# Optimization experiments

Hardware: AMD Instinct MI355X
Metric: run time of the kernel (lower is better)

The kernel has to match this reference:

```python
import jax, jax.numpy as jnp
from jax import lax
import numpy as np
import math

B_SZ, SEQ, D_MODEL = 2, 2048, 2048
D_INNER, D_STATE, D_CONV, HEADS, P, CHUNK = 4096, 128, 4, 64, 64, 128
CONV_DIM = D_INNER + 2 * D_STATE
D_IN_PROJ = 2 * D_INNER + 2 * D_STATE + HEADS


def setup_inputs() -> dict:
    key = jax.random.key(0)
    ks = jax.random.split(key, 6)
    hidden_states = jax.random.normal(ks[0], (B_SZ, SEQ, D_MODEL), jnp.float32)
    W_in = jax.random.normal(ks[1], (D_IN_PROJ, D_MODEL), jnp.float32) * 0.02
    W_conv = jax.random.normal(ks[2], (CONV_DIM, 1, D_CONV), jnp.float32) * 0.2
    b_conv = jnp.zeros((CONV_DIM,), jnp.float32)
    A_log = jnp.log(jnp.arange(1, HEADS + 1, dtype=jnp.float32))
    D = jnp.ones((HEADS,), jnp.float32)
    # dt_bias init as in the torch module
    dt = jnp.exp(jax.random.uniform(ks[3], (HEADS,)) * (math.log(0.1) - math.log(0.001)) + math.log(0.001))
    dt = jnp.clip(dt, 1e-4, None)
    dt_bias = dt + jnp.log(-jnp.expm1(-dt))
    norm_weight = jnp.ones((D_INNER,), jnp.float32)
    W_out = jax.random.normal(ks[4], (D_MODEL, D_INNER), jnp.float32) * 0.02
    return {"hidden_states": hidden_states, "W_in": W_in, "W_conv": W_conv, "b_conv": b_conv,
            "A_log": A_log, "D": D, "dt_bias": dt_bias, "norm_weight": norm_weight, "W_out": W_out}


def _mamba2_core(hidden_states, W_in, W_conv, b_conv, A_log, D, dt_bias, norm_weight, W_out):
    Bsz, L, _ = hidden_states.shape
    NC = L // CHUNK
    zxbcdt = hidden_states @ W_in.T                         # [B,L,d_in_proj]
    z = zxbcdt[..., :D_INNER]
    xBC = zxbcdt[..., D_INNER:D_INNER + CONV_DIM]
    dt = zxbcdt[..., -HEADS:]
    # causal depthwise conv1d over sequence
    xc = jnp.swapaxes(xBC, 1, 2)                            # [B,C,L]
    xc = lax.conv_general_dilated(xc, W_conv, (1,), [(D_CONV - 1, 0)],
                                  feature_group_count=CONV_DIM,
                                  dimension_numbers=('NCH', 'OIH', 'NCH'))
    xc = xc + b_conv[None, :, None]
    xBC = jax.nn.silu(jnp.swapaxes(xc, 1, 2))               # [B,L,conv_dim]
    x = xBC[..., :D_INNER]
    Bm = xBC[..., D_INNER:D_INNER + D_STATE]                # num_groups=1
    Cm = xBC[..., -D_STATE:]
    dt = jax.nn.softplus(dt + dt_bias)                      # [B,L,H]; dt_limit (0,inf) is a no-op
    A = -jnp.exp(A_log)                                     # [H]
    # --- chunked SSD scan (chunk_size = CHUNK), same math as torch_ssm ---
    xch = x.reshape(Bsz, NC, CHUNK, HEADS, P)
    dtc = dt.reshape(Bsz, NC, CHUNK, HEADS)
    Bc = Bm.reshape(Bsz, NC, CHUNK, D_STATE)
    Cc = Cm.reshape(Bsz, NC, CHUNK, D_STATE)
    u = xch * dtc[..., None]                                # [b,c,l,h,p]
    dA = dtc * A                                            # [b,c,l,h]
    dA_cs = jnp.cumsum(dA, axis=2)                          # [b,c,l,h]
    # within-chunk causal attention-like term
    seg = dA_cs[:, :, :, None, :] - dA_cs[:, :, None, :, :] # [b,c,l,s,h]
    mask = jnp.tril(jnp.ones((CHUNK, CHUNK), bool))
    Lmat = jnp.exp(jnp.where(mask[None, None, :, :, None], seg, -jnp.inf))
    CB = jnp.einsum('bcln,bcsn->bcls', Cc, Bc)
    M = CB[..., None] * Lmat                                # [b,c,l,s,h]
    Y_diag = jnp.einsum('bclsh,bcshp->bclhp', M, u)
    # per-chunk final states
    decay_states = jnp.exp(dA_cs[:, :, -1:, :] - dA_cs)     # [b,c,l,h]
    states = jnp.einsum('bcln,bclh,bclhp->bchpn', Bc, decay_states, u)
    chunk_decay = jnp.exp(dA_cs[:, :, -1, :])               # [b,c,h]
    # inter-chunk recurrence over NC chunks
    def step(h, inp):
        st, cd = inp                                        # [b,h,p,n], [b,h]
        h_new = h * cd[:, :, None, None] + st
        return h_new, h                                     # emit state at chunk start
    sts = jnp.moveaxis(states, 1, 0)
    cds = jnp.moveaxis(chunk_decay, 1, 0)
    h0 = jnp.zeros((Bsz, HEADS, P, D_STATE), hidden_states.dtype)
    _, h_starts = lax.scan(step, h0, (sts, cds))
    h_starts = jnp.moveaxis(h_starts, 0, 1)                 # [b,c,h,p,n]
    state_decay_out = jnp.exp(dA_cs)                        # [b,c,l,h]
    Y_off = jnp.einsum('bcln,bclh,bchpn->bclhp', Cc, state_decay_out, h_starts)
    Y = Y_diag + Y_off + D[None, None, None, :, None] * xch
    y = Y.reshape(Bsz, L, D_INNER)
    # gated RMSNorm (gate first, then norm; group_size == d_inner)
    yg = y * jax.nn.silu(z)
    var = jnp.mean(yg * yg, axis=-1, keepdims=True)
    y = yg * lax.rsqrt(var + 1e-5) * norm_weight
    return y @ W_out.T


def reference(hidden_states, W_in, W_conv, b_conv, A_log, D, dt_bias, norm_weight, W_out):
    return _mamba2_core(hidden_states, W_in, W_conv, b_conv, A_log, D, dt_bias, norm_weight, W_out)
```

## Files before the change

### kernel.cpp

```cpp
#include <hip/hip_runtime.h>
#include <hip/hip_bf16.h>
#include <stdint.h>

typedef __bf16 bf16;
typedef __bf16 bf16x8 __attribute__((ext_vector_type(8)));
typedef __bf16 bf16x4 __attribute__((ext_vector_type(4)));
typedef float f32x4v __attribute__((ext_vector_type(4)));

#define SEQ    2048
#define DMODEL 2048
#define DI     4096
#define NH     64
#define PDIM   64
#define CHUNKL 128
#define NCH    16
#define CONVD  4352
#define DPROJ  8512
#define ZLD    8704
#define NTOK   4096
#define LP     136

__device__ __forceinline__ float sigmoid_f(float x){ return 1.f/(1.f+expf(-x)); }
__device__ __forceinline__ float silu_f(float x){ return x*sigmoid_f(x); }
__device__ __forceinline__ float softplus_f(float x){ return x > 20.f ? x : log1pf(expf(x)); }

__global__ __launch_bounds__(256) void cvt_all_kernel(const float* __restrict__ hs,
                                                      const float* __restrict__ W_in,
                                                      const float* __restrict__ W_out,
                                                      bf16* __restrict__ hsb,
                                                      bf16* __restrict__ winb,
                                                      bf16* __restrict__ woutb){
    int blk = blockIdx.x;
    if (blk < 8192){
        int i = (blk*256 + threadIdx.x)*4;
        float4 v = *(const float4*)&hs[i];
        bf16x4 o; o[0]=(bf16)v.x; o[1]=(bf16)v.y; o[2]=(bf16)v.z; o[3]=(bf16)v.w;
        *(bf16x4*)&hsb[i] = o;
    } else if (blk < 25600){
        int i = ((blk-8192)*256 + threadIdx.x)*4;
        int r = i >> 11;
        bf16x4 o;
        if (r < DPROJ){
            float4 v = *(const float4*)&W_in[i];
            o[0]=(bf16)v.x; o[1]=(bf16)v.y; o[2]=(bf16)v.z; o[3]=(bf16)v.w;
        } else {
            o[0]=(bf16)0.f; o[1]=(bf16)0.f; o[2]=(bf16)0.f; o[3]=(bf16)0.f;
        }
        *(bf16x4*)&winb[i] = o;
    } else {
        int i = ((blk-25600)*256 + threadIdx.x)*4;
        float4 v = *(const float4*)&W_out[i];
        bf16x4 o; o[0]=(bf16)v.x; o[1]=(bf16)v.y; o[2]=(bf16)v.z; o[3]=(bf16)v.w;
        *(bf16x4*)&woutb[i] = o;
    }
}

#define READ_AF(BUFP, QM, AF)                                                          \
    {                                                                                  \
        _Pragma("unroll")                                                              \
        for (int i=0;i<4;i++)                                                          \
            _Pragma("unroll")                                                          \
            for (int k2=0;k2<2;k2++)                                                   \
                AF[i][k2] = *(const bf16x8*)&(BUFP)[aoff[i][k2] + (QM)*8192];          \
    }

#define READ_B(BUFP, QN, BFR)                                                          \
    {                                                                                  \
        _Pragma("unroll")                                                              \
        for (int nf=0;nf<2;nf++)                                                       \
            _Pragma("unroll")                                                          \
            for (int k2=0;k2<2;k2++)                                                   \
                BFR[nf][k2] = *(const bf16x8*)&(BUFP)[boff[nf][k2] + (QN)*8192];       \
    }

#define MMA_QA(AF, QM, QN, BFR)                                                        \
    {                                                                                  \
        __builtin_amdgcn_s_setprio(1);                                                 \
        _Pragma("unroll")                                                              \
        for (int i=0;i<4;i++)                                                          \
            _Pragma("unroll")                                                          \
            for (int nf=0;nf<2;nf++)                                                   \
                _Pragma("unroll")                                                      \
                for (int k2=0;k2<2;k2++)                                               \
                    acc[(QM)*4+i][(QN)*2+nf] = __builtin_amdgcn_mfma_f32_16x16x32_bf16( \
                        AF[i][k2], BFR[nf][k2], acc[(QM)*4+i][(QN)*2+nf], 0,0,0);      \
        __builtin_amdgcn_s_setprio(0);                                                 \
    }

#define SBAR() do { __builtin_amdgcn_sched_barrier(0);                                 \
                    __builtin_amdgcn_s_barrier();                                      \
                    asm volatile("s_waitcnt lgkmcnt(0)" ::: "memory");                 \
                    __builtin_amdgcn_sched_barrier(0); } while(0)

__global__ __launch_bounds__(512) void gemm1_kernel(const bf16* __restrict__ A,
                                                    const bf16* __restrict__ Bmat,
                                                    bf16* __restrict__ Cz,
                                                    float* __restrict__ tpart,
                                                    int NXB, int NYB, int K){
    __shared__ __align__(16) bf16 lds[2][2*16384];
    const int tid  = threadIdx.x;
    const int w    = tid >> 6;
    const int lane = tid & 63;
    const int wm   = w >> 2, wn = w & 3;
    const int bid  = blockIdx.x;

    int aoff[4][2], boff[2][2];
    #pragma unroll
    for (int i=0;i<4;i++)
        #pragma unroll
        for (int k2=0;k2<2;k2++){
            int ra0 = wm*64 + i*16 + (lane&15);
            int slot = (k2*4 + (lane>>4)) ^ (ra0&7);
            aoff[i][k2] = ra0*64 + slot*8;
        }
    #pragma unroll
    for (int nf=0;nf<2;nf++)
        #pragma unroll
        for (int k2=0;k2<2;k2++){
            int rb0 = wn*32 + nf*16 + (lane&15);
            int slot = (k2*4 + (lane>>4)) ^ (rb0&7);
            boff[nf][k2] = 16384 + rb0*64 + slot*8;
        }
    const int er = (lane>>4)*4, ec = lane&15;

    if (bid < 256){
        int kz  = bid >> 6;
        int t64 = bid & 63;
        const int tn2 = 8192 + (t64 & 3)*128;
        const int tm2 = (t64 >> 2)*256;
        const int kt0 = kz*8;

        const bf16* srcA2[2][2];
        const bf16* srcB2[2];
        #pragma unroll
        for (int r0h=0;r0h<2;r0h++)
            #pragma unroll
            for (int i=0;i<2;i++){
                int lr = r0h*128 + i*64 + (tid>>3);
                int growA = tm2 + ((lr>>6)&1)*128 + (lr>>7)*64 + (lr&63);
                int gslot = (tid&7) ^ (lr&7);
                srcA2[r0h][i] = A + (long)growA*K + gslot*8;
            }
        #pragma unroll
        for (int i=0;i<2;i++){
            int lr = i*64 + (tid>>3);
            int gslot = (tid&7) ^ (lr&7);
            srcB2[i] = Bmat + (long)(tn2 + lr)*K + gslot*8;
        }
        auto stA = [&](int buf, int t, int r0h){
            long koff = (long)(kt0 + t)*64;
            #pragma unroll
            for (int i=0;i<2;i++){
                bf16* dst = &lds[buf][0] + (size_t)(r0h*128 + i*64 + w*8)*64;
                __builtin_amdgcn_global_load_lds(
                    (const __attribute__((address_space(1))) void*)(srcA2[r0h][i] + koff),
                    (__attribute__((address_space(3))) void*)dst, 16, 0, 0);
            }
        };
        auto stB = [&](int buf, int t){
            long koff = (long)(kt0 + t)*64;
            #pragma unroll
            for (int i=0;i<2;i++){
                bf16* dst = &lds[buf][16384] + (size_t)(i*64 + w*8)*64;
                __builtin_amdgcn_global_load_lds(
                    (const __attribute__((address_space(1))) void*)(srcB2[i] + koff),
                    (__attribute__((address_space(3))) void*)dst, 16, 0, 0);
            }
        };

        f32x4v acc2[8][2];
        #pragma unroll
        for (int i=0;i<8;i++)
            #pragma unroll
            for (int j=0;j<2;j++) acc2[i][j] = {0.f,0.f,0.f,0.f};
        bf16x8 af[4][2], af1[4][2], bfr0[2][2];

        stA(0,0,0); stA(0,0,1); stB(0,0);
        __syncthreads();
        int cur = 0;
        for (int t=0; t<8; ++t){
            int nxt = cur ^ 1;
            const bf16* bufc = &lds[cur][0];
            if (t+1 < 8){ stA(nxt,t+1,0); stA(nxt,t+1,1); stB(nxt,t+1); }
            READ_AF(bufc, 0, af)
            READ_AF(bufc, 1, af1)
            READ_B(bufc, 0, bfr0)
            #pragma unroll
            for (int i=0;i<4;i++)
                #pragma unroll
                for (int nf=0;nf<2;nf++)
                    #pragma unroll
                    for (int k2=0;k2<2;k2++)
                        acc2[i][nf] = __builtin_amdgcn_mfma_f32_16x16x32_bf16(
                            af[i][k2], bfr0[nf][k2], acc2[i][nf], 0,0,0);
            #pragma unroll
            for (int i=0;i<4;i++)
                #pragma unroll
                for (int nf=0;nf<2;nf++)
                    #pragma unroll
                    for (int k2=0;k2<2;k2++)
                        acc2[4+i][nf] = __builtin_amdgcn_mfma_f32_16x16x32_bf16(
                            af1[i][k2], bfr0[nf][k2], acc2[4+i][nf], 0,0,0);
            __syncthreads();
            cur = nxt;
        }
        #pragma unroll
        for (int mi=0;mi<8;mi++)
            #pragma unroll
            for (int nf=0;nf<2;nf++){
                long r0 = tm2 + wm*128 + mi*16 + er;
                int  c0 = tn2 + wn*32 + nf*16 + ec;
                #pragma unroll
                for (int j=0;j<4;j++)
                    tpart[((long)kz*4096 + (r0+j))*512 + (c0 - 8192)] = acc2[mi][nf][j];
            }
        return;
    }

    int bid2 = bid - 256;
    int wg   = (bid2 & 7)*64 + (bid2 >> 3);
    const int SW = 8;
    int sup = wg / (SW*NYB);
    int rr  = wg % (SW*NYB);
    int x0  = sup*SW;
    int wl  = (NXB - x0 < SW) ? (NXB - x0) : SW;
    int x   = x0 + rr % wl;
    int y   = rr / wl;
    const int tm = y*256, tn = x*256;
    const int KT = K >> 6;

    f32x4v acc[8][4];
    #pragma unroll
    for (int i=0;i<8;i++)
        #pragma unroll
        for (int j=0;j<4;j++) acc[i][j] = {0.f,0.f,0.f,0.f};
    bf16x8 af[4][2], af1[4][2];
    bf16x8 bfr0[2][2], bfr1[2][2];

    const bf16* srcA[2][2];
    const bf16* srcB[2][2];
    #pragma unroll
    for (int r0h=0;r0h<2;r0h++)
        #pragma unroll
        for (int i=0;i<2;i++){
            int lr = r0h*128 + i*64 + (tid>>3);
            int growA = tm + ((lr>>6)&1)*128 + (lr>>7)*64 + (lr&63);
            int growB = tn + ((lr>>5)&3)*64 + (lr>>7)*32 + (lr&31);
            int gslot = (tid&7) ^ (lr&7);
            srcA[r0h][i] = A + (long)growA*K + gslot*8;
            srcB[r0h][i] = Bmat + (long)growB*K + gslot*8;
        }

    auto stageA = [&](int buf, int t, int r0h){
        long koff = (long)t*64;
        #pragma unroll
        for (int i=0;i<2;i++){
            bf16* dst = &lds[buf][0] + (size_t)(r0h*128 + i*64 + w*8)*64;
            __builtin_amdgcn_global_load_lds(
                (const __attribute__((address_space(1))) void*)(srcA[r0h][i] + koff),
                (__attribute__((address_space(3))) void*)dst, 16, 0, 0);
        }
    };
    auto stageB = [&](int buf, int t, int r0h){
        long koff = (long)t*64;
        #pragma unroll
        for (int i=0;i<2;i++){
            bf16* dst = &lds[buf][16384] + (size_t)(r0h*128 + i*64 + w*8)*64;
            __builtin_amdgcn_global_load_lds(
                (const __attribute__((address_space(1))) void*)(srcB[r0h][i] + koff),
                (__attribute__((address_space(3))) void*)dst, 16, 0, 0);
        }
    };

    stageA(0, 0, 0); stageB(0, 0, 0); stageB(0, 0, 1); stageA(0, 0, 1);
    if (KT > 1){ stageA(1, 1, 0); stageB(1, 1, 0); stageB(1, 1, 1); }

    int cur = 0;
    for (int t = 0; t < KT; ++t){
        int nxt = cur ^ 1;
        const bf16* bufc = &lds[cur][0];
        if (t+1 < KT){ asm volatile("s_waitcnt vmcnt(6)" ::: "memory"); }
        else         { asm volatile("s_waitcnt vmcnt(0)" ::: "memory"); }
        __builtin_amdgcn_sched_barrier(0);
        __builtin_amdgcn_s_barrier();
        __builtin_amdgcn_sched_barrier(0);
        if (t+1 < KT) stageA(nxt, t+1, 1);
        READ_AF(bufc, 0, af)
        READ_AF(bufc, 1, af1)
        READ_B(bufc, 0, bfr0)
        READ_B(bufc, 1, bfr1)
        asm volatile("s_waitcnt lgkmcnt(0)" ::: "memory");
        __builtin_amdgcn_sched_barrier(0);
        MMA_QA(af, 0, 0, bfr0)
        MMA_QA(af, 0, 1, bfr1)
        __builtin_amdgcn_sched_barrier(0);
        __builtin_amdgcn_s_barrier();
        __builtin_amdgcn_sched_barrier(0);
        if (t+2 < KT){ stageA(cur, t+2, 0); stageB(cur, t+2, 0); stageB(cur, t+2, 1); }
        MMA_QA(af1, 1, 0, bfr0)
        MMA_QA(af1, 1, 1, bfr1)
        __builtin_amdgcn_sched_barrier(0);
        cur = nxt;
    }

    #pragma unroll
    for (int mi=0;mi<8;mi++)
        #pragma unroll
        for (int ni=0;ni<4;ni++){
            long r0 = tm + wm*128 + mi*16 + er;
            int  c0 = tn + wn*64 + ni*16 + ec;
            #pragma unroll
            for (int j=0;j<4;j++)
                Cz[(r0+j)*ZLD + c0] = (bf16)acc[mi][ni][j];
        }
}

__global__ __launch_bounds__(512) void gemm256x128_kernel(const bf16* __restrict__ A,
                                                          const bf16* __restrict__ Bmat,
                                                          float* __restrict__ C,
                                                          int NXB, int NYB, int K, int ldc){
    __shared__ __align__(16) bf16 lds[3][24576];
    const int tid  = threadIdx.x;
    const int w    = tid >> 6;
    const int lane = tid & 63;
    const int wm   = w >> 2, wn = w & 3;

    int bid = blockIdx.x, nb = gridDim.x;
    int wg = (bid & 7)*(nb >> 3) + (bid >> 3);
    const int SW = 8;
    int sup = wg / (SW*NYB);
    int rr  = wg % (SW*NYB);
    int x0  = sup*SW;
    int wl  = (NXB - x0 < SW) ? (NXB - x0) : SW;
    int x   = x0 + rr % wl;
    int y   = rr / wl;
    const int tm = y*256, tn = x*128;
    const int KT = K >> 6;

    f32x4v acc[8][2];
    #pragma unroll
    for (int i=0;i<8;i++)
        #pragma unroll
        for (int j=0;j<2;j++) acc[i][j] = {0.f,0.f,0.f,0.f};
    bf16x8 af[4][2], af1[4][2];
    bf16x8 bfr[2][2];

    const bf16* srcA[2][2];
    const bf16* srcB[2];
    #pragma unroll
    for (int r0h=0;r0h<2;r0h++)
        #pragma unroll
        for (int i=0;i<2;i++){
            int lr = r0h*128 + i*64 + (tid>>3);
            int growA = tm + ((lr>>6)&1)*128 + (lr>>7)*64 + (lr&63);
            int gslot = (tid&7) ^ (lr&7);
            srcA[r0h][i] = A + (long)growA*K + gslot*8;
        }
    #pragma unroll
    for (int i=0;i<2;i++){
        int lr = i*64 + (tid>>3);
        int gslot = (tid&7) ^ (lr&7);
        srcB[i] = Bmat + (long)(tn + lr)*K + gslot*8;
    }
    int aoff[4][2], boff[2][2];
    #pragma unroll
    for (int i=0;i<4;i++)
        #pragma unroll
        for (int k2=0;k2<2;k2++){
            int ra0 = wm*64 + i*16 + (lane&15);
            int slot = (k2*4 + (lane>>4)) ^ (ra0&7);
            aoff[i][k2] = ra0*64 + slot*8;
        }
    #pragma unroll
    for (int nf=0;nf<2;nf++)
        #pragma unroll
        for (int k2=0;k2<2;k2++){
            int rb0 = wn*32 + nf*16 + (lane&15);
            int slot = (k2*4 + (lane>>4)) ^ (rb0&7);
            boff[nf][k2] = 16384 + rb0*64 + slot*8;
        }

    auto stageA = [&](int buf, int t, int r0h){
        long koff = (long)t*64;
        #pragma unroll
        for (int i=0;i<2;i++){
            bf16* dst = &lds[buf][0] + (size_t)(r0h*128 + i*64 + w*8)*64;
            __builtin_amdgcn_global_load_lds(
                (const __attribute__((address_space(1))) void*)(srcA[r0h][i] + koff),
                (__attribute__((address_space(3))) void*)dst, 16, 0, 0);
        }
    };
    auto stageB = [&](int buf, int t){
        long koff = (long)t*64;
        #pragma unroll
        for (int i=0;i<2;i++){
            bf16* dst = &lds[buf][16384] + (size_t)(i*64 + w*8)*64;
            __builtin_amdgcn_global_load_lds(
                (const __attribute__((address_space(1))) void*)(srcB[i] + koff),
                (__attribute__((address_space(3))) void*)dst, 16, 0, 0);
        }
    };

    stageA(0, 0, 0); stageA(0, 0, 1); stageB(0, 0);
    if (KT > 1){ stageA(1, 1, 0); stageA(1, 1, 1); stageB(1, 1); }
    asm volatile("s_waitcnt vmcnt(6)" ::: "memory");
    __builtin_amdgcn_s_barrier();

    int cur = 0;
    for (int t = 0; t < KT; ++t){
        int stb = cur + 2; if (stb >= 3) stb -= 3;
        const bf16* bufc = &lds[cur][0];
        READ_AF(bufc, 0, af)
        READ_AF(bufc, 1, af1)
        READ_B(bufc, 0, bfr)
        if (t+2 < KT){ stageA(stb, t+2, 0); stageA(stb, t+2, 1); }
        SBAR();
        MMA_QA(af, 0, 0, bfr)
        if (t+2 < KT){
            stageB(stb, t+2);
            asm volatile("s_waitcnt vmcnt(6)" ::: "memory");
        } else {
            asm volatile("s_waitcnt vmcnt(0)" ::: "memory");
        }
        SBAR();
        MMA_QA(af1, 1, 0, bfr)
        cur = (cur == 2) ? 0 : cur + 1;
    }

    const int er = (lane>>4)*4, ec = lane&15;
    #pragma unroll
    for (int mi=0;mi<8;mi++)
        #pragma unroll
        for (int ni=0;ni<2;ni++){
            long r0 = tm + wm*128 + mi*16 + er;
            int  c0 = tn + wn*32 + ni*16 + ec;
            #pragma unroll
            for (int j=0;j<4;j++)
                C[(r0+j)*ldc + c0] = acc[mi][ni][j];
        }
}

__global__ __launch_bounds__(256) void tailreduce_kernel(const float* __restrict__ p,
                                                         bf16* __restrict__ zx,
                                                         float* __restrict__ dtf){
    long i = ((long)blockIdx.x*256 + threadIdx.x)*4;
    int r = (int)(i >> 9);
    int c = (int)(i & 511);
    const long Q = (long)4096*512;
    float4 a  = *(const float4*)&p[i];
    float4 b  = *(const float4*)&p[i+Q];
    float4 cc = *(const float4*)&p[i+2*Q];
    float4 d  = *(const float4*)&p[i+3*Q];
    float s0 = a.x+b.x+cc.x+d.x, s1 = a.y+b.y+cc.y+d.y;
    float s2 = a.z+b.z+cc.z+d.z, s3 = a.w+b.w+cc.w+d.w;
    bf16x4 o; o[0]=(bf16)s0; o[1]=(bf16)s1; o[2]=(bf16)s2; o[3]=(bf16)s3;
    *(bf16x4*)&zx[(long)r*ZLD + 8192 + c] = o;
    int col = 8192 + c;
    float sv[4] = {s0,s1,s2,s3};
    #pragma unroll
    for (int j=0;j<4;j++){
        int cj = col + j;
        if (cj >= 8448 && cj < 8512) dtf[(long)r*64 + (cj-8448)] = sv[j];
    }
}

__global__ __launch_bounds__(256) void mid1_kernel(const bf16* __restrict__ zx,
                                                   const float* __restrict__ Wc,
                                                   const float* __restrict__ bc,
                                                   const float* __restrict__ dtf,
                                                   const float* __restrict__ A_log,
                                                   const float* __restrict__ dt_bias,
                                                   bf16* __restrict__ xc,
                                                   float* __restrict__ dtv,
                                                   float* __restrict__ dacs,
                                                   float* __restrict__ cdec){
    int blk = blockIdx.x;
    if (blk < 2560){
        int by = blk/5, bx = blk%5;
        int c4 = bx*256 + threadIdx.x;
        if (c4 >= 1088) return;
        int ch = c4*4;
        int b = by >> 8, t0 = (by & 255)*8;
        float4 tap[4];
        #pragma unroll
        for (int e=0;e<4;e++) tap[e] = *(const float4*)&Wc[(ch+e)*4];
        float4 bq = *(const float4*)&bc[ch];
        float bca[4] = {bq.x, bq.y, bq.z, bq.w};
        const bf16* col = zx + (long)(b*SEQ)*ZLD + 4096 + ch;
        bf16x4 v[11];
        #pragma unroll
        for (int k=0;k<11;k++){
            int t = t0 - 3 + k;
            if (t >= 0) v[k] = *(const bf16x4*)&col[(long)t*ZLD];
            else { v[k][0]=(bf16)0.f; v[k][1]=(bf16)0.f; v[k][2]=(bf16)0.f; v[k][3]=(bf16)0.f; }
        }
        #pragma unroll
        for (int j=0;j<8;j++){
            bf16x4 o;
            #pragma unroll
            for (int e=0;e<4;e++){
                float acc = bca[e] + (float)v[j][e]*tap[e].x + (float)v[j+1][e]*tap[e].y
                                   + (float)v[j+2][e]*tap[e].z + (float)v[j+3][e]*tap[e].w;
                o[e] = (bf16)silu_f(acc);
            }
            *(bf16x4*)&xc[(long)(b*SEQ + t0 + j)*CONVD + ch] = o;
        }
    } else {
        int wid  = ((blk-2560)*256 + threadIdx.x) >> 6;
        int lane = threadIdx.x & 63;
        int h  = wid & 63, bc2 = wid >> 6;
        int b  = bc2 >> 4,  c  = bc2 & 15;
        float Ah   = -expf(A_log[h]);
        float bias = dt_bias[h];
        long tok0 = (long)(b*SEQ + c*CHUNKL);
        int l0 = lane*2;
        float d0 = softplus_f(dtf[(tok0+l0)*64 + h] + bias);
        float d1 = softplus_f(dtf[(tok0+l0+1)*64 + h] + bias);
        float s = (d0 + d1)*Ah;
        #pragma unroll
        for (int off=1; off<64; off<<=1){
            float t = __shfl_up(s, off, 64);
            if (lane >= off) s += t;
        }
        long base_h = (long)wid*128;
        float cs1 = s;
        float cs0 = s - d1*Ah;
        dtv[base_h+l0]   = d0;  dtv[base_h+l0+1]  = d1;
        dacs[base_h+l0]  = cs0; dacs[base_h+l0+1] = cs1;
        if (lane == 63) cdec[wid] = expf(cs1);
    }
}

__global__ __launch_bounds__(256) void cb_mfma_kernel(const bf16* __restrict__ xc,
                                                      float* __restrict__ cb,
                                                      bf16* __restrict__ BT){
    __shared__ __align__(16) bf16 A1[128*LP];
    __shared__ __align__(16) bf16 B1[128*LP];
    int blk = blockIdx.x;  int b = blk>>4, c = blk&15;
    int tid = threadIdx.x;
    const int w = tid >> 6, lane = tid & 63;
    long tok0 = (long)(b*SEQ + c*CHUNKL);
    int l = tid>>1, n0 = (tid&1)*64;
    const bf16* crow = xc + tok0*CONVD + (long)l*CONVD;
    #pragma unroll
    for (int v=0;v<8;v++){
        *(bf16x8*)&A1[l*LP + n0 + v*8] = *(const bf16x8*)&crow[4224 + n0 + v*8];
        *(bf16x8*)&B1[l*LP + n0 + v*8] = *(const bf16x8*)&crow[4096 + n0 + v*8];
    }
    __syncthreads();
    f32x4v acc[2][8];
    #pragma unroll
    for (int mi=0;mi<2;mi++)
        #pragma unroll
        for (int ni=0;ni<8;ni++) acc[mi][ni] = {0.f,0.f,0.f,0.f};
    #pragma unroll
    for (int kk=0; kk<128; kk+=32){
        bf16x8 afr[2], bfr2[8];
        #pragma unroll
        for (int mi=0;mi<2;mi++)
            afr[mi] = *(const bf16x8*)&A1[(w*32 + mi*16 + (lane&15))*LP + kk + (lane>>4)*8];
        #pragma unroll
        for (int ni=0;ni<8;ni++)
            bfr2[ni] = *(const bf16x8*)&B1[(ni*16 + (lane&15))*LP + kk + (lane>>4)*8];
        #pragma unroll
        for (int mi=0;mi<2;mi++)
            #pragma unroll
            for (int ni=0;ni<8;ni++)
                acc[mi][ni] = __builtin_amdgcn_mfma_f32_16x16x32_bf16(afr[mi], bfr2[ni], acc[mi][ni], 0,0,0);
    }
    float* out = cb + (long)blk*16384;
    #pragma unroll
    for (int mi=0;mi<2;mi++)
        #pragma unroll
        for (int ni=0;ni<8;ni++){
            int r0 = w*32 + mi*16 + (lane>>4)*4;
            int c0 = ni*16 + (lane&15);
            #pragma unroll
            for (int j=0;j<4;j++) out[(long)(r0+j)*128 + c0] = acc[mi][ni][j];
        }
    {
        int n = tid>>1, s0 = (tid&1)*64;
        bf16* btp = BT + (long)blk*16384 + (long)n*128 + s0;
        #pragma unroll
        for (int v=0;v<8;v++){
            bf16x8 o;
            #pragma unroll
            for (int e=0;e<8;e++) o[e] = B1[(s0+v*8+e)*LP + n];
            *(bf16x8*)&btp[v*8] = o;
        }
    }
}

__global__ __launch_bounds__(256) void states_mfma_kernel(const bf16* __restrict__ xc,
                                                          const bf16* __restrict__ BT,
                                                          const float* __restrict__ dtv,
                                                          const float* __restrict__ dacs,
                                                          bf16* __restrict__ states){
    __shared__ __align__(16) bf16 A1[64*LP];
    __shared__ __align__(16) bf16 B1[128*LP];
    __shared__ float wgtl[128];
    int blk = blockIdx.x;
    int h = blk & 63, bc = blk >> 6;
    int b = bc >> 4, c = bc & 15;
    int tid = threadIdx.x;
    const int w = tid >> 6, lane = tid & 63;
    long tok0 = (long)(b*SEQ + c*CHUNKL);
    long base_h = (long)blk*128;
    float cs_last = dacs[base_h + 127];
    if (tid < 128) wgtl[tid] = dtv[base_h+tid] * expf(cs_last - dacs[base_h+tid]);
    __syncthreads();
    #pragma unroll
    for (int t=0;t<4;t++){
        int l = (tid>>3) + t*32;
        int p0 = (tid&7)*8;
        bf16x8 xv = *(const bf16x8*)&xc[(tok0+l)*CONVD + h*64 + p0];
        float wv = wgtl[l];
        #pragma unroll
        for (int e=0;e<8;e++) A1[(p0+e)*LP + l] = (bf16)((float)xv[e]*wv);
    }
    {
        int n = tid>>1, l0 = (tid&1)*64;
        const bf16* btp = BT + (long)bc*16384 + (long)n*128 + l0;
        #pragma unroll
        for (int v=0;v<8;v++)
            *(bf16x8*)&B1[n*LP + l0 + v*8] = *(const bf16x8*)&btp[v*8];
    }
    __syncthreads();
    f32x4v acc[8];
    #pragma unroll
    for (int ni=0;ni<8;ni++) acc[ni] = {0.f,0.f,0.f,0.f};
    #pragma unroll
    for (int kk=0; kk<128; kk+=32){
        bf16x8 afr = *(const bf16x8*)&A1[(w*16 + (lane&15))*LP + kk + (lane>>4)*8];
        #pragma unroll
        for (int ni=0;ni<8;ni++){
            bf16x8 bfr2 = *(const bf16x8*)&B1[(ni*16 + (lane&15))*LP + kk + (lane>>4)*8];
            acc[ni] = __builtin_amdgcn_mfma_f32_16x16x32_bf16(afr, bfr2, acc[ni], 0,0,0);
        }
    }
    bf16* out = states + (long)blk*8192;
    #pragma unroll
    for (int ni=0;ni<8;ni++){
        int p0 = w*16 + (lane>>4)*4;
        int n  = ni*16 + (lane&15);
        #pragma unroll
        for (int j=0;j<4;j++) out[(long)(p0+j)*128 + n] = (bf16)acc[ni][j];
    }
}

__global__ __launch_bounds__(256) void scan_kernel(const bf16* __restrict__ states,
                                                   const float* __restrict__ cdec,
                                                   bf16* __restrict__ hst){
    long gid = (long)blockIdx.x*256 + threadIdx.x;
    int n = gid & 127;
    int p = (gid >> 7) & 63;
    int h = (gid >> 13) & 63;
    int b = (int)(gid >> 19);
    float hrun = 0.f;
    for (int c=0;c<16;c++){
        long idx = ((((long)(b*16 + c)*64 + h)*64 + p)*128) + n;
        hst[idx] = (bf16)hrun;
        hrun = hrun * cdec[(b*16+c)*64 + h] + (float)states[idx];
    }
}

__global__ __launch_bounds__(256) void yfused_kernel(const bf16* __restrict__ xc,
                                                     const float* __restrict__ cb,
                                                     const bf16* __restrict__ hst,
                                                     const float* __restrict__ dtv,
                                                     const float* __restrict__ dacs,
                                                     bf16* __restrict__ Ybf){
    __shared__ __align__(16) bf16 A1[128*LP];
    __shared__ __align__(16) bf16 B1[64*LP];
    __shared__ float csl[128];
    int blk = blockIdx.x;
    int h = blk & 63, bc = blk >> 6;
    int b = bc >> 4, c = bc & 15;
    int tid = threadIdx.x;
    const int w = tid >> 6, lane = tid & 63;
    long tok0 = (long)(b*SEQ + c*CHUNKL);
    long base_h = (long)blk*128;
    if (tid < 128) csl[tid] = dacs[base_h + tid];
    __syncthreads();
    {
        int l = tid>>1, s0 = (tid&1)*64;
        float el = csl[l];
        const float* cbrow = cb + (long)bc*16384 + (long)l*128 + s0;
        int jend = l - s0; if (jend > 63) jend = 63;
        for (int j=0; j<=jend; j++)
            A1[l*LP + s0 + j] = (bf16)(cbrow[j]*expf(el - csl[s0+j]));
        for (int j=jend+1; j<64; j++)
            A1[l*LP + s0 + j] = (bf16)0.f;
    }
    #pragma unroll
    for (int t=0;t<4;t++){
        int s = (tid>>3) + t*32;
        int p0 = (tid&7)*8;
        bf16x8 xv = *(const bf16x8*)&xc[(tok0+s)*CONVD + h*64 + p0];
        float wv = dtv[base_h + s];
        #pragma unroll
        for (int e=0;e<8;e++) B1[(p0+e)*LP + s] = (bf16)((float)xv[e]*wv);
    }
    __syncthreads();
    f32x4v acc[2][4];
    #pragma unroll
    for (int mi=0;mi<2;mi++)
        #pragma unroll
        for (int ni=0;ni<4;ni++) acc[mi][ni] = {0.f,0.f,0.f,0.f};
    #pragma unroll
    for (int kk=0; kk<128; kk+=32){
        bf16x8 afr[2], bfr2[4];
        #pragma unroll
        for (int mi=0;mi<2;mi++)
            afr[mi] = *(const bf16x8*)&A1[(w*32 + mi*16 + (lane&15))*LP + kk + (lane>>4)*8];
        #pragma unroll
        for (int ni=0;ni<4;ni++)
            bfr2[ni] = *(const bf16x8*)&B1[(ni*16 + (lane&15))*LP + kk + (lane>>4)*8];
        #pragma unroll
        for (int mi=0;mi<2;mi++)
            #pragma unroll
            for (int ni=0;ni<4;ni++)
                acc[mi][ni] = __builtin_amdgcn_mfma_f32_16x16x32_bf16(afr[mi], bfr2[ni], acc[mi][ni], 0,0,0);
    }
    __syncthreads();
    {
        int l = tid>>1, n0 = (tid&1)*64;
        float e1 = expf(csl[l]);
        const bf16* crow = xc + (tok0+l)*CONVD + 4224;
        #pragma unroll
        for (int v=0;v<8;v++){
            bf16x8 cv = *(const bf16x8*)&crow[n0 + v*8];
            bf16x8 o;
            #pragma unroll
            for (int e=0;e<8;e++) o[e] = (bf16)((float)cv[e]*e1);
            *(bf16x8*)&A1[l*LP + n0 + v*8] = o;
        }
    }
    {
        int p = tid>>2, n0 = (tid&3)*32;
        const bf16* hrow = hst + (long)blk*8192 + (long)p*128 + n0;
        #pragma unroll
        for (int v=0;v<4;v++)
            *(bf16x8*)&B1[p*LP + n0 + v*8] = *(const bf16x8*)&hrow[v*8];
    }
    __syncthreads();
    #pragma unroll
    for (int kk=0; kk<128; kk+=32){
        bf16x8 afr[2], bfr2[4];
        #pragma unroll
        for (int mi=0;mi<2;mi++)
            afr[mi] = *(const bf16x8*)&A1[(w*32 + mi*16 + (lane&15))*LP + kk + (lane>>4)*8];
        #pragma unroll
        for (int ni=0;ni<4;ni++)
            bfr2[ni] = *(const bf16x8*)&B1[(ni*16 + (lane&15))*LP + kk + (lane>>4)*8];
        #pragma unroll
        for (int mi=0;mi<2;mi++)
            #pragma unroll
            for (int ni=0;ni<4;ni++)
                acc[mi][ni] = __builtin_amdgcn_mfma_f32_16x16x32_bf16(afr[mi], bfr2[ni], acc[mi][ni], 0,0,0);
    }
    #pragma unroll
    for (int mi=0;mi<2;mi++)
        #pragma unroll
        for (int ni=0;ni<4;ni++){
            int l0 = w*32 + mi*16 + (lane>>4)*4;
            int p  = ni*16 + (lane&15);
            #pragma unroll
            for (int j=0;j<4;j++)
                Ybf[(tok0 + l0 + j)*DI + h*64 + p] = (bf16)acc[mi][ni][j];
        }
}

__global__ __launch_bounds__(256) void gatenorm_kernel(const bf16* __restrict__ Ybf,
                                                       const bf16* __restrict__ zx,
                                                       const bf16* __restrict__ xc,
                                                       const float* __restrict__ Dp,
                                                       const float* __restrict__ nw,
                                                       bf16* __restrict__ ybn){
    __shared__ float red[4];
    int tok = blockIdx.x, tid = threadIdx.x;
    const bf16* yrow = Ybf + (long)tok*DI;
    const bf16* zrow = zx  + (long)tok*ZLD;
    const bf16* xrow = xc  + (long)tok*CONVD;
    float yg[16];
    float ss = 0.f;
    #pragma unroll
    for (int k=0;k<2;k++){
        int d = (tid + k*256)*8;
        bf16x8 yv = *(const bf16x8*)&yrow[d];
        bf16x8 zv = *(const bf16x8*)&zrow[d];
        bf16x8 xv = *(const bf16x8*)&xrow[d];
        float dh = Dp[d>>6];
        #pragma unroll
        for (int e=0;e<8;e++){
            float yy = (float)yv[e] + dh*(float)xv[e];
            float g = yy*silu_f((float)zv[e]);
            yg[k*8+e] = g;
            ss += g*g;
        }
    }
    #pragma unroll
    for (int off=32; off>0; off>>=1) ss += __shfl_down(ss, off, 64);
    if ((tid & 63) == 0) red[tid>>6] = ss;
    __syncthreads();
    float tot = red[0]+red[1]+red[2]+red[3];
    float scale = rsqrtf(tot/(float)DI + 1e-5f);
    #pragma unroll
    for (int k=0;k<2;k++){
        int d = (tid + k*256)*8;
        float4 w0 = *(const float4*)&nw[d];
        float4 w1 = *(const float4*)&nw[d+4];
        float wv[8] = {w0.x,w0.y,w0.z,w0.w,w1.x,w1.y,w1.z,w1.w};
        bf16x8 o;
        #pragma unroll
        for (int e=0;e<8;e++) o[e] = (bf16)(yg[k*8+e]*scale*wv[e]);
        *(bf16x8*)&ybn[(long)tok*DI + d] = o;
    }
}

extern "C" void kernel_launch(void* const* d_in, const int* in_sizes, int n_in,
                              void* d_out, int out_size, void* d_ws, size_t ws_size,
                              hipStream_t stream){
    const float* hs      = (const float*)d_in[0];
    const float* W_in    = (const float*)d_in[1];
    const float* W_conv  = (const float*)d_in[2];
    const float* b_conv  = (const float*)d_in[3];
    const float* A_log   = (const float*)d_in[4];
    const float* Dp      = (const float*)d_in[5];
    const float* dt_bias = (const float*)d_in[6];
    const float* nw      = (const float*)d_in[7];
    const float* W_out   = (const float*)d_in[8];
    float* out = (float*)d_out;

    char* ws = (char*)d_ws;
    const size_t OFF_ZX    = 0;
    const size_t OFF_DTF   = 71303168;
    const size_t OFF_XC    = 72351744;
    const size_t OFF_DTV   = 108003328;
    const size_t OFF_DACS  = 109051904;
    const size_t OFF_CDEC  = 110100480;
    const size_t OFF_CB    = 110108672;
    const size_t OFF_SLOTA = 112205824;
    const size_t OFF_SLOTB = 179314688;
    const size_t OFF_WOUTB = 212869120;

    bf16*  zx    = (bf16*)(ws + OFF_ZX);
    float* dtf   = (float*)(ws + OFF_DTF);
    bf16*  xc    = (bf16*)(ws + OFF_XC);
    float* dtv   = (float*)(ws + OFF_DTV);
    float* dacs  = (float*)(ws + OFF_DACS);
    float* cdec  = (float*)(ws + OFF_CDEC);
    float* cbuf  = (float*)(ws + OFF_CB);
    bf16*  hsb   = (bf16*)(ws + OFF_SLOTA);
    bf16*  winb  = (bf16*)(ws + OFF_SLOTA + 16777216);
    bf16*  states= (bf16*)(ws + OFF_SLOTA);
    bf16*  Ybf   = (bf16*)(ws + OFF_SLOTA);
    float* tpart = (float*)(ws + OFF_SLOTB);
    bf16*  BTb   = (bf16*)(ws + OFF_SLOTB);
    bf16*  hst   = (bf16*)(ws + OFF_SLOTB);
    bf16*  ybn   = (bf16*)(ws + OFF_SLOTB);
    bf16*  woutb = (bf16*)(ws + OFF_WOUTB);

    cvt_all_kernel<<<33792, 256, 0, stream>>>(hs, W_in, W_out, hsb, winb, woutb);

    gemm1_kernel<<<768, 512, 0, stream>>>(hsb, winb, zx, tpart, 32, 16, DMODEL);
    tailreduce_kernel<<<2048, 256, 0, stream>>>(tpart, zx, dtf);

    mid1_kernel<<<3072, 256, 0, stream>>>(zx, W_conv, b_conv, dtf, A_log, dt_bias,
                                          xc, dtv, dacs, cdec);
    cb_mfma_kernel<<<32, 256, 0, stream>>>(xc, cbuf, BTb);
    states_mfma_kernel<<<2048, 256, 0, stream>>>(xc, BTb, dtv, dacs, states);
    scan_kernel<<<4096, 256, 0, stream>>>(states, cdec, hst);
    yfused_kernel<<<2048, 256, 0, stream>>>(xc, cbuf, hst, dtv, dacs, Ybf);
    gatenorm_kernel<<<4096, 256, 0, stream>>>(Ybf, zx, xc, Dp, nw, ybn);

    gemm256x128_kernel<<<256, 512, 0, stream>>>(ybn, woutb, out, 16, 16, DI, DMODEL);
}
```

Measured before the change: 381.7 us.

## Replace split-K tail GEMM with uniform 128x256 tiled in-projection GEMM

The in-projection GEMM previously used 256x256 tiles for the main columns plus a split-K path for the 512-column tail, whose partial sums were reduced by a separate tail kernel. It is now one uniform kernel with 128x256 tiles, K-step 32, and a smaller LDS footprint allowing up to 4 blocks per CU. The dt columns go straight to dtf in fp32 from the epilogue. This removes the split-K partial-sum round trip and one kernel launch, but uses smaller tiles with less reuse per block and twice as many K iterations.

Result: slower. 407.5 us (+6.8%).

```diff
diff --git a/kernel.cpp b/kernel.cpp
--- a/kernel.cpp
+++ b/kernel.cpp
@@ -55,6 +55,128 @@
     }
 }
 
+__global__ __launch_bounds__(512, 4) void gemm1_kernel(const bf16* __restrict__ A,
+                                                       const bf16* __restrict__ Bmat,
+                                                       bf16* __restrict__ Cz,
+                                                       float* __restrict__ dtf,
+                                                       int NXB, int NYB, int K){
+    __shared__ __align__(16) bf16 lds[2][12288];
+    const int tid  = threadIdx.x;
+    const int w    = tid >> 6;
+    const int lane = tid & 63;
+    const int wm   = w >> 2, wn = w & 3;
+
+    int bid = blockIdx.x, nb = gridDim.x;
+    int wg  = (bid & 7)*(nb >> 3) + (bid >> 3);
+    const int SW = 8;
+    int sup = wg / (SW*NYB);
+    int rr  = wg % (SW*NYB);
+    int x0  = sup*SW;
+    int wl  = (NXB - x0 < SW) ? (NXB - x0) : SW;
+    int x   = x0 + rr % wl;
+    int y   = rr / wl;
+    const int tm = y*128, tn = x*256;
+    const int KT = K >> 5;
+
+    f32x4v acc[4][4];
+    #pragma unroll
+    for (int i=0;i<4;i++)
+        #pragma unroll
+        for (int j=0;j<4;j++) acc[i][j] = {0.f,0.f,0.f,0.f};
+    bf16x8 af[4], bfr[4];
+
+    const bf16* srcA1;
+    const bf16* srcB2[2];
+    {
+        int row = tid >> 2;
+        int gslot = (tid & 3) ^ ((row >> 1) & 3);
+        srcA1 = A + (long)(tm + row)*K + gslot*8;
+        #pragma unroll
+        for (int i=0;i<2;i++){
+            int rb = i*128 + row;
+            int gs = (tid & 3) ^ ((rb >> 1) & 3);
+            srcB2[i] = Bmat + (long)(tn + rb)*K + gs*8;
+        }
+    }
+    int aoff[4], boff[4];
+    #pragma unroll
+    for (int mi=0;mi<4;mi++){
+        int ra = wm*64 + mi*16 + (lane&15);
+        int slot = (lane>>4) ^ ((ra>>1)&3);
+        aoff[mi] = ra*32 + slot*8;
+    }
+    #pragma unroll
+    for (int ni=0;ni<4;ni++){
+        int rb = wn*64 + ni*16 + (lane&15);
+        int slot = (lane>>4) ^ ((rb>>1)&3);
+        boff[ni] = 4096 + rb*32 + slot*8;
+    }
+
+    auto stage = [&](int buf, int t){
+        long koff = (long)t*32;
+        {
+            bf16* dst = &lds[buf][0] + (size_t)w*512;
+            __builtin_amdgcn_global_load_lds(
+                (const __attribute__((address_space(1))) void*)(srcA1 + koff),
+                (__attribute__((address_space(3))) void*)dst, 16, 0, 0);
+        }
+        #pragma unroll
+        for (int i=0;i<2;i++){
+            bf16* dst = &lds[buf][4096] + (size_t)(i*4096 + w*512);
+            __builtin_amdgcn_global_load_lds(
+                (const __attribute__((address_space(1))) void*)(srcB2[i] + koff),
+                (__attribute__((address_space(3))) void*)dst, 16, 0, 0);
+        }
+    };
+
+    stage(0, 0);
+    if (KT > 1) stage(1, 1);
+
+    int cur = 0;
+    for (int t = 0; t < KT; ++t){
+        const bf16* bufc = &lds[cur][0];
+        if (t+1 < KT){ asm volatile("s_waitcnt vmcnt(3)" ::: "memory"); }
+        else         { asm volatile("s_waitcnt vmcnt(0)" ::: "memory"); }
+        __builtin_amdgcn_sched_barrier(0);
+        __builtin_amdgcn_s_barrier();
+        __builtin_amdgcn_sched_barrier(0);
+        #pragma unroll
+        for (int mi=0;mi<4;mi++) af[mi]  = *(const bf16x8*)&bufc[aoff[mi]];
+        #pragma unroll
+        for (int ni=0;ni<4;ni++) bfr[ni] = *(const bf16x8*)&bufc[boff[ni]];
+        asm volatile("s_waitcnt lgkmcnt(0)" ::: "memory");
+        __builtin_amdgcn_sched_barrier(0);
+        __builtin_amdgcn_s_setprio(1);
+        #pragma unroll
+        for (int mi=0;mi<4;mi++)
+            #pragma unroll
+            for (int ni=0;ni<4;ni++)
+                acc[mi][ni] = __builtin_amdgcn_mfma_f32_16x16x32_bf16(af[mi], bfr[ni], acc[mi][ni], 0,0,0);
+        __builtin_amdgcn_s_setprio(0);
+        __builtin_amdgcn_sched_barrier(0);
+        __builtin_amdgcn_s_barrier();
+        __builtin_amdgcn_sched_barrier(0);
+        if (t+2 < KT) stage(cur, t+2);
+        cur ^= 1;
+    }
+
+    const int er = (lane>>4)*4, ec = lane&15;
+    #pragma unroll
+    for (int mi=0;mi<4;mi++)
+        #pragma unroll
+        for (int ni=0;ni<4;ni++){
+            long r0 = tm + wm*64 + mi*16 + er;
+            int  c0 = tn + wn*64 + ni*16 + ec;
+            #pragma unroll
+            for (int j=0;j<4;j++){
+                float val = acc[mi][ni][j];
+                Cz[(r0+j)*ZLD + c0] = (bf16)val;
+                if (c0 >= 8448 && c0 < 8512)
+                    dtf[(r0+j)*64 + (c0 - 8448)] = val;
+            }
+        }
+}
+
 #define READ_AF(BUFP, QM, AF)                                                          \
     {                                                                                  \
         _Pragma("unroll")                                                              \
@@ -91,229 +213,6 @@
                     __builtin_amdgcn_s_barrier();                                      \
                     asm volatile("s_waitcnt lgkmcnt(0)" ::: "memory");                 \
                     __builtin_amdgcn_sched_barrier(0); } while(0)
-
-__global__ __launch_bounds__(512) void gemm1_kernel(const bf16* __restrict__ A,
-                                                    const bf16* __restrict__ Bmat,
-                                                    bf16* __restrict__ Cz,
-                                                    float* __restrict__ tpart,
-                                                    int NXB, int NYB, int K){
-    __shared__ __align__(16) bf16 lds[2][2*16384];
-    const int tid  = threadIdx.x;
-    const int w    = tid >> 6;
-    const int lane = tid & 63;
-    const int wm   = w >> 2, wn = w & 3;
-    const int bid  = blockIdx.x;
-
-    int aoff[4][2], boff[2][2];
-    #pragma unroll
-    for (int i=0;i<4;i++)
-        #pragma unroll
-        for (int k2=0;k2<2;k2++){
-            int ra0 = wm*64 + i*16 + (lane&15);
-            int slot = (k2*4 + (lane>>4)) ^ (ra0&7);
-            aoff[i][k2] = ra0*64 + slot*8;
-        }
-    #pragma unroll
-    for (int nf=0;nf<2;nf++)
-        #pragma unroll
-        for (int k2=0;k2<2;k2++){
-            int rb0 = wn*32 + nf*16 + (lane&15);
-            int slot = (k2*4 + (lane>>4)) ^ (rb0&7);
-            boff[nf][k2] = 16384 + rb0*64 + slot*8;
-        }
-    const int er = (lane>>4)*4, ec = lane&15;
-
-    if (bid < 256){
-        int kz  = bid >> 6;
-        int t64 = bid & 63;
-        const int tn2 = 8192 + (t64 & 3)*128;
-        const int tm2 = (t64 >> 2)*256;
-        const int kt0 = kz*8;
-
-        const bf16* srcA2[2][2];
-        const bf16* srcB2[2];
-        #pragma unroll
-        for (int r0h=0;r0h<2;r0h++)
-            #pragma unroll
-            for (int i=0;i<2;i++){
-                int lr = r0h*128 + i*64 + (tid>>3);
-                int growA = tm2 + ((lr>>6)&1)*128 + (lr>>7)*64 + (lr&63);
-                int gslot = (tid&7) ^ (lr&7);
-                srcA2[r0h][i] = A + (long)growA*K + gslot*8;
-            }
-        #pragma unroll
-        for (int i=0;i<2;i++){
-            int lr = i*64 + (tid>>3);
-            int gslot = (tid&7) ^ (lr&7);
-            srcB2[i] = Bmat + (long)(tn2 + lr)*K + gslot*8;
-        }
-        auto stA = [&](int buf, int t, int r0h){
-            long koff = (long)(kt0 + t)*64;
-            #pragma unroll
-            for (int i=0;i<2;i++){
-                bf16* dst = &lds[buf][0] + (size_t)(r0h*128 + i*64 + w*8)*64;
-                __builtin_amdgcn_global_load_lds(
-                    (const __attribute__((address_space(1))) void*)(srcA2[r0h][i] + koff),
-                    (__attribute__((address_space(3))) void*)dst, 16, 0, 0);
-            }
-        };
-        auto stB = [&](int buf, int t){
-            long koff = (long)(kt0 + t)*64;
-            #pragma unroll
-            for (int i=0;i<2;i++){
-                bf16* dst = &lds[buf][16384] + (size_t)(i*64 + w*8)*64;
-                __builtin_amdgcn_global_load_lds(
-                    (const __attribute__((address_space(1))) void*)(srcB2[i] + koff),
-                    (__attribute__((address_space(3))) void*)dst, 16, 0, 0);
-            }
-        };
-
-        f32x4v acc2[8][2];
-        #pragma unroll
-        for (int i=0;i<8;i++)
-            #pragma unroll
-            for (int j=0;j<2;j++) acc2[i][j] = {0.f,0.f,0.f,0.f};
-        bf16x8 af[4][2], af1[4][2], bfr0[2][2];
-
-        stA(0,0,0); stA(0,0,1); stB(0,0);
-        __syncthreads();
-        int cur = 0;
-        for (int t=0; t<8; ++t){
-            int nxt = cur ^ 1;
-            const bf16* bufc = &lds[cur][0];
-            if (t+1 < 8){ stA(nxt,t+1,0); stA(nxt,t+1,1); stB(nxt,t+1); }
-            READ_AF(bufc, 0, af)
-            READ_AF(bufc, 1, af1)
-            READ_B(bufc, 0, bfr0)
-            #pragma unroll
-            for (int i=0;i<4;i++)
-                #pragma unroll
-                for (int nf=0;nf<2;nf++)
-                    #pragma unroll
-                    for (int k2=0;k2<2;k2++)
-                        acc2[i][nf] = __builtin_amdgcn_mfma_f32_16x16x32_bf16(
-                            af[i][k2], bfr0[nf][k2], acc2[i][nf], 0,0,0);
-            #pragma unroll
-            for (int i=0;i<4;i++)
-                #pragma unroll
-                for (int nf=0;nf<2;nf++)
-                    #pragma unroll
-                    for (int k2=0;k2<2;k2++)
-                        acc2[4+i][nf] = __builtin_amdgcn_mfma_f32_16x16x32_bf16(
-                            af1[i][k2], bfr0[nf][k2], acc2[4+i][nf], 0,0,0);
-            __syncthreads();
-            cur = nxt;
-        }
-        #pragma unroll
-        for (int mi=0;mi<8;mi++)
-            #pragma unroll
-            for (int nf=0;nf<2;nf++){
-                long r0 = tm2 + wm*128 + mi*16 + er;
-                int  c0 = tn2 + wn*32 + nf*16 + ec;
-                #pragma unroll
-                for (int j=0;j<4;j++)
-                    tpart[((long)kz*4096 + (r0+j))*512 + (c0 - 8192)] = acc2[mi][nf][j];
-            }
-        return;
-    }
-
-    int bid2 = bid - 256;
-    int wg   = (bid2 & 7)*64 + (bid2 >> 3);
-    const int SW = 8;
-    int sup = wg / (SW*NYB);
-    int rr  = wg % (SW*NYB);
-    int x0  = sup*SW;
-    int wl  = (NXB - x0 < SW) ? (NXB - x0) : SW;
-    int x   = x0 + rr % wl;
-    int y   = rr / wl;
-    const int tm = y*256, tn = x*256;
-    const int KT = K >> 6;
-
-    f32x4v acc[8][4];
-    #pragma unroll
-    for (int i=0;i<8;i++)
-        #pragma unroll
-        for (int j=0;j<4;j++) acc[i][j] = {0.f,0.f,0.f,0.f};
-    bf16x8 af[4][2], af1[4][2];
-    bf16x8 bfr0[2][2], bfr1[2][2];
-
-    const bf16* srcA[2][2];
-    const bf16* srcB[2][2];
-    #pragma unroll
-    for (int r0h=0;r0h<2;r0h++)
-        #pragma unroll
-        for (int i=0;i<2;i++){
-            int lr = r0h*128 + i*64 + (tid>>3);
-            int growA = tm + ((lr>>6)&1)*128 + (lr>>7)*64 + (lr&63);
-            int growB = tn + ((lr>>5)&3)*64 + (lr>>7)*32 + (lr&31);
-            int gslot = (tid&7) ^ (lr&7);
-            srcA[r0h][i] = A + (long)growA*K + gslot*8;
-            srcB[r0h][i] = Bmat + (long)growB*K + gslot*8;
-        }
-
-    auto stageA = [&](int buf, int t, int r0h){
-        long koff = (long)t*64;
-        #pragma unroll
-        for (int i=0;i<2;i++){
-            bf16* dst = &lds[buf][0] + (size_t)(r0h*128 + i*64 + w*8)*64;
-            __builtin_amdgcn_global_load_lds(
-                (const __attribute__((address_space(1))) void*)(srcA[r0h][i] + koff),
-                (__attribute__((address_space(3))) void*)dst, 16, 0, 0);
-        }
-    };
-    auto stageB = [&](int buf, int t, int r0h){
-        long koff = (long)t*64;
-        #pragma unroll
-        for (int i=0;i<2;i++){
-            bf16* dst = &lds[buf][16384] + (size_t)(r0h*128 + i*64 + w*8)*64;
-            __builtin_amdgcn_global_load_lds(
-                (const __attribute__((address_space(1))) void*)(srcB[r0h][i] + koff),
-                (__attribute__((address_space(3))) void*)dst, 16, 0, 0);
-        }
-    };
-
-    stageA(0, 0, 0); stageB(0, 0, 0); stageB(0, 0, 1); stageA(0, 0, 1);
-    if (KT > 1){ stageA(1, 1, 0); stageB(1, 1, 0); stageB(1, 1, 1); }
-
-    int cur = 0;
-    for (int t = 0; t < KT; ++t){
-        int nxt = cur ^ 1;
-        const bf16* bufc = &lds[cur][0];
-        if (t+1 < KT){ asm volatile("s_waitcnt vmcnt(6)" ::: "memory"); }
-        else         { asm volatile("s_waitcnt vmcnt(0)" ::: "memory"); }
-        __builtin_amdgcn_sched_barrier(0);
-        __builtin_amdgcn_s_barrier();
-        __builtin_amdgcn_sched_barrier(0);
-        if (t+1 < KT) stageA(nxt, t+1, 1);
-        READ_AF(bufc, 0, af)
-        READ_AF(bufc, 1, af1)
-        READ_B(bufc, 0, bfr0)
-        READ_B(bufc, 1, bfr1)
-        asm volatile("s_waitcnt lgkmcnt(0)" ::: "memory");
-        __builtin_amdgcn_sched_barrier(0);
-        MMA_QA(af, 0, 0, bfr0)
-        MMA_QA(af, 0, 1, bfr1)
-        __builtin_amdgcn_sched_barrier(0);
-        __builtin_amdgcn_s_barrier();
-        __builtin_amdgcn_sched_barrier(0);
-        if (t+2 < KT){ stageA(cur, t+2, 0); stageB(cur, t+2, 0); stageB(cur, t+2, 1); }
-        MMA_QA(af1, 1, 0, bfr0)
-        MMA_QA(af1, 1, 1, bfr1)
-        __builtin_amdgcn_sched_barrier(0);
-        cur = nxt;
-    }
-
-    #pragma unroll
-    for (int mi=0;mi<8;mi++)
-        #pragma unroll
-        for (int ni=0;ni<4;ni++){
-            long r0 = tm + wm*128 + mi*16 + er;
-            int  c0 = tn + wn*64 + ni*16 + ec;
-            #pragma unroll
-            for (int j=0;j<4;j++)
-                Cz[(r0+j)*ZLD + c0] = (bf16)acc[mi][ni][j];
-        }
-}
 
 __global__ __launch_bounds__(512) void gemm256x128_kernel(const bf16* __restrict__ A,
                                                           const bf16* __restrict__ Bmat,
@@ -438,30 +337,6 @@
             for (int j=0;j<4;j++)
                 C[(r0+j)*ldc + c0] = acc[mi][ni][j];
         }
-}
-
-__global__ __launch_bounds__(256) void tailreduce_kernel(const float* __restrict__ p,
-                                                         bf16* __restrict__ zx,
-                                                         float* __restrict__ dtf){
-    long i = ((long)blockIdx.x*256 + threadIdx.x)*4;
-    int r = (int)(i >> 9);
-    int c = (int)(i & 511);
-    const long Q = (long)4096*512;
-    float4 a  = *(const float4*)&p[i];
-    float4 b  = *(const float4*)&p[i+Q];
-    float4 cc = *(const float4*)&p[i+2*Q];
-    float4 d  = *(const float4*)&p[i+3*Q];
-    float s0 = a.x+b.x+cc.x+d.x, s1 = a.y+b.y+cc.y+d.y;
-    float s2 = a.z+b.z+cc.z+d.z, s3 = a.w+b.w+cc.w+d.w;
-    bf16x4 o; o[0]=(bf16)s0; o[1]=(bf16)s1; o[2]=(bf16)s2; o[3]=(bf16)s3;
-    *(bf16x4*)&zx[(long)r*ZLD + 8192 + c] = o;
-    int col = 8192 + c;
-    float sv[4] = {s0,s1,s2,s3};
-    #pragma unroll
-    for (int j=0;j<4;j++){
-        int cj = col + j;
-        if (cj >= 8448 && cj < 8512) dtf[(long)r*64 + (cj-8448)] = sv[j];
-    }
 }
 
 __global__ __launch_bounds__(256) void mid1_kernel(const bf16* __restrict__ zx,
@@ -855,7 +730,6 @@
     bf16*  winb  = (bf16*)(ws + OFF_SLOTA + 16777216);
     bf16*  states= (bf16*)(ws + OFF_SLOTA);
     bf16*  Ybf   = (bf16*)(ws + OFF_SLOTA);
-    float* tpart = (float*)(ws + OFF_SLOTB);
     bf16*  BTb   = (bf16*)(ws + OFF_SLOTB);
     bf16*  hst   = (bf16*)(ws + OFF_SLOTB);
     bf16*  ybn   = (bf16*)(ws + OFF_SLOTB);
@@ -863,8 +737,7 @@
 
     cvt_all_kernel<<<33792, 256, 0, stream>>>(hs, W_in, W_out, hsb, winb, woutb);
 
-    gemm1_kernel<<<768, 512, 0, stream>>>(hsb, winb, zx, tpart, 32, 16, DMODEL);
-    tailreduce_kernel<<<2048, 256, 0, stream>>>(tpart, zx, dtf);
+    gemm1_kernel<<<1088, 512, 0, stream>>>(hsb, winb, zx, dtf, 34, 32, DMODEL);
 
     mid1_kernel<<<3072, 256, 0, stream>>>(zx, W_conv, b_conv, dtf, A_log, dt_bias,
                                           xc, dtv, dacs, cdec);
```
